# Kernel optimization log

Hardware: AMD Instinct MI355X
Metric: run time of the kernel (lower is better)

The kernel has to match this reference:

```python
import jax, jax.numpy as jnp
import numpy as np

EMBED_DIM = 768

def setup_inputs() -> dict:
    key = jax.random.key(0)
    ks = jax.random.split(key, 5)
    C = EMBED_DIM
    x = jax.random.normal(ks[0], (32, 1024, C), dtype=jnp.float32)
    s = 1.0 / np.sqrt(C)
    W_qkv = jax.random.normal(ks[1], (C, 3 * C), dtype=jnp.float32) * s
    b_qkv = jnp.zeros((3 * C,), dtype=jnp.float32)
    W_proj = jax.random.normal(ks[2], (C, C), dtype=jnp.float32) * s
    b_proj = jnp.zeros((C,), dtype=jnp.float32)
    return {"x": x, "W_qkv": W_qkv, "b_qkv": b_qkv, "W_proj": W_proj, "b_proj": b_proj}

def reference(x, W_qkv, b_qkv, W_proj, b_proj):
    B, N, C = x.shape
    qkv = x @ W_qkv + b_qkv                      # [B, N, 3C]
    q, k, v = jnp.split(qkv, 3, axis=-1)         # each [B, N, C]
    scale = 1.0 / jnp.sqrt(jnp.asarray(C, dtype=x.dtype))
    attn = jnp.einsum('bnc,bmc->bnm', q, k) * scale  # [B, N, N]
    attn = jax.nn.softmax(attn, axis=-1)
    out = jnp.einsum('bnm,bmc->bnc', attn, v)    # [B, N, C]
    return out @ W_proj + b_proj
```

## Files before the change

### kernel.cpp

```cpp
#include <hip/hip_runtime.h>

typedef __bf16 bf16;
typedef __bf16 bf16x4 __attribute__((ext_vector_type(4)));
typedef __bf16 bf16x8 __attribute__((ext_vector_type(8)));
typedef float f32x4 __attribute__((ext_vector_type(4)));

constexpr int BATCH = 32;
constexpr int SEQ   = 1024;
constexpr int CDIM  = 768;
constexpr int ROWS  = BATCH * SEQ;
constexpr int QKVC  = 3 * CDIM;

constexpr size_t oWqT = 0;
constexpr size_t oWpT = oWqT + (size_t)QKVC * CDIM * 2;
constexpr size_t oQKV = oWpT + (size_t)CDIM * CDIM * 2;
constexpr size_t oS   = oQKV + (size_t)ROWS * QKVC * 2;
constexpr size_t oVT  = oS   + (size_t)BATCH * SEQ * SEQ * 2;
constexpr size_t oInv = oVT  + (size_t)BATCH * CDIM * SEQ * 2;
constexpr size_t oAO  = oQKV;
constexpr size_t oXB  = oS;
constexpr size_t oPart= oWqT;

__device__ __forceinline__ void gld_lds16(const void* g, void* l) {
  __builtin_amdgcn_global_load_lds(
      (const __attribute__((address_space(1))) unsigned int*)g,
      (__attribute__((address_space(3))) unsigned int*)l,
      16, 0, 0);
}

__global__ __launch_bounds__(256) void f2b_kernel(const float* __restrict__ x,
                                                  bf16* __restrict__ y) {
  int i = blockIdx.x * blockDim.x + threadIdx.x;
  const float* p = x + (size_t)i * 8;
  float4 a = *(const float4*)p;
  float4 b = *(const float4*)(p + 4);
  bf16x8 o;
  o[0]=(bf16)a.x; o[1]=(bf16)a.y; o[2]=(bf16)a.z; o[3]=(bf16)a.w;
  o[4]=(bf16)b.x; o[5]=(bf16)b.y; o[6]=(bf16)b.z; o[7]=(bf16)b.w;
  *(bf16x8*)(y + (size_t)i * 8) = o;
}

__global__ __launch_bounds__(256) void wt_kernel(const float* __restrict__ W,
                                                 bf16* __restrict__ T, int N) {
  __shared__ float t[32][33];
  int k0 = blockIdx.x * 32, n0 = blockIdx.y * 32;
  int tx = threadIdx.x & 31, ty = threadIdx.x >> 5;
  #pragma unroll
  for (int i = 0; i < 4; ++i)
    t[ty + i * 8][tx] = W[(size_t)(k0 + ty + i * 8) * N + n0 + tx];
  __syncthreads();
  #pragma unroll
  for (int i = 0; i < 4; ++i)
    T[(size_t)(n0 + ty + i * 8) * 768 + k0 + tx] = (bf16)t[tx][ty + i * 8];
}

__global__ __launch_bounds__(256) void finish_kernel(const float* __restrict__ partial,
                                                     float* __restrict__ inv) {
  int i = blockIdx.x * 256 + threadIdx.x;
  float4 p = *(const float4*)(partial + (size_t)i * 4);
  inv[i] = 1.0f / (p.x + p.y + p.z + p.w);
}


#define DSRD_A(dst_, qm_) do {                                                   \
  _Pragma("unroll")                                                              \
  for (int i_ = 0; i_ < 4; ++i_) {                                               \
    const int row_ = wm * 128 + (qm_) * 64 + i_ * 16 + lr;                       \
    const char* rb_ = (const char*)Acur + row_ * 128;                            \
    dst_[i_][0] = *(const bf16x8*)(rb_ + ((0  + kb0) ^ swz));                    \
    dst_[i_][1] = *(const bf16x8*)(rb_ + ((64 + kb0) ^ swz));                    \
  }                                                                              \
} while (0)

#define DSRD_B(dst_, qn_) do {                                                   \
  _Pragma("unroll")                                                              \
  for (int j_ = 0; j_ < 2; ++j_) {                                               \
    const int row_ = wn * 64 + (qn_) * 32 + j_ * 16 + lr;                        \
    const char* rb_ = (const char*)Bcur + row_ * 128;                            \
    dst_[j_][0] = *(const bf16x8*)(rb_ + ((0  + kb0) ^ swz));                    \
    dst_[j_][1] = *(const bf16x8*)(rb_ + ((64 + kb0) ^ swz));                    \
  }                                                                              \
} while (0)

#define STG_A(buf_, kt_, h_) do {                                                \
  gld_lds16(Ast + (size_t)((h_) * 128 +  0) * lda + (size_t)(kt_) * 64,          \
            &LDSB[(buf_)][((h_) * 2 + 0) * 4096 + wv * 512]);                    \
  gld_lds16(Ast + (size_t)((h_) * 128 + 64) * lda + (size_t)(kt_) * 64,          \
            &LDSB[(buf_)][((h_) * 2 + 1) * 4096 + wv * 512]);                    \
} while (0)

#define STG_B(buf_, kt_, h_) do {                                                \
  gld_lds16(Bst + (size_t)((h_) * 128 +  0) * ldb + (size_t)(kt_) * 64,          \
            &LDSB[2 + (buf_)][((h_) * 2 + 0) * 4096 + wv * 512]);                \
  gld_lds16(Bst + (size_t)((h_) * 128 + 64) * ldb + (size_t)(kt_) * 64,          \
            &LDSB[2 + (buf_)][((h_) * 2 + 1) * 4096 + wv * 512]);                \
} while (0)

#define MMA16(a_, b_, mo_, no_) do {                                             \
  asm volatile("s_waitcnt lgkmcnt(0)" ::: "memory");                             \
  __builtin_amdgcn_sched_barrier(0);                                             \
  __builtin_amdgcn_s_setprio(1);                                                 \
  _Pragma("unroll")                                                              \
  for (int ks_ = 0; ks_ < 2; ++ks_)                                              \
    _Pragma("unroll")                                                            \
    for (int i_ = 0; i_ < 4; ++i_)                                               \
      _Pragma("unroll")                                                          \
      for (int j_ = 0; j_ < 2; ++j_)                                             \
        acc[(mo_) + i_][(no_) + j_] =                                            \
            __builtin_amdgcn_mfma_f32_16x16x32_bf16(a_[i_][ks_], b_[j_][ks_],    \
                acc[(mo_) + i_][(no_) + j_], 0, 0, 0);                           \
  __builtin_amdgcn_s_setprio(0);                                                 \
} while (0)

#define PIN() __builtin_amdgcn_sched_barrier(0)
#define BAR() __builtin_amdgcn_s_barrier()

template<bool OUT_BF16, bool HAS_BIAS, bool ROW_SCALE, bool FUSE_EXP, bool TR_V>
__global__ __launch_bounds__(512, 2) void gemm256(
    const bf16* __restrict__ Ap, const bf16* __restrict__ Bp, void* __restrict__ Cp,
    int K, int lda, int ldb, int ldc, int ntm, int ntn,
    long sA, long sB, long sC,
    float scale, const float* __restrict__ rowScale, long sRS,
    const float* __restrict__ bias, float* __restrict__ partial,
    bf16* __restrict__ vtout)
{
  __shared__ __align__(16) bf16 LDSB[4][256 * 64];
  const int tid  = threadIdx.x;
  const int lane = tid & 63;
  const int wv   = tid >> 6;
  const int wm   = wv >> 2;
  const int wn   = wv & 3;

  const int total = (int)gridDim.x;
  const int chunk = total >> 3;
  const int bid   = (int)blockIdx.x;
  int sbid = (bid & 7) * chunk + (bid >> 3);
  const int pb = ntm * ntn;
  const int z  = sbid / pb;  sbid -= z * pb;
  const int mt = sbid / ntn;
  const int nt = sbid - mt * ntn;
  const int m0 = mt * 256, n0 = nt * 256;

  const bf16* A = Ap + (size_t)z * sA;
  const bf16* B = Bp + (size_t)z * sB;

  const int sr  = tid >> 3;
  const int sc8 = tid & 7;
  const int gch = sc8 ^ (sr & 7);
  const bf16* Ast = A + (size_t)(m0 + sr) * lda + gch * 8;
  const bf16* Bst = B + (size_t)(n0 + sr) * ldb + gch * 8;

  const int lr  = lane & 15;
  const int swz = (lane & 7) << 4;
  const int kb0 = (lane >> 4) * 16;

  f32x4 acc[8][4] = {};
  const int nkt = K >> 6;

  STG_A(0, 0, 0); STG_A(0, 0, 1);
  STG_B(0, 0, 0); STG_B(0, 0, 1);
  if (nkt > 1) { STG_A(1, 1, 0); STG_A(1, 1, 1); }

  bf16x8 a0[4][2], a1[4][2], b0[2][2], b1[2][2];
  for (int t = 0; t < nkt; ++t) {
    const int cur = t & 1;
    const bf16* Acur = LDSB[cur];
    const bf16* Bcur = LDSB[2 + cur];
    const bool sb = (t + 1 < nkt);
    const bool sa = (t + 2 < nkt);
    if (sa) asm volatile("s_waitcnt vmcnt(4)" ::: "memory");
    else    asm volatile("s_waitcnt vmcnt(0)" ::: "memory");
    BAR(); PIN();
    DSRD_A(a0, 0); DSRD_B(b0, 0);
    PIN();
    if (sb) STG_B(cur ^ 1, t + 1, 0);
    MMA16(a0, b0, 0, 0);
    DSRD_A(a1, 1);
    PIN();
    if (sb) STG_B(cur ^ 1, t + 1, 1);
    MMA16(a1, b0, 4, 0);
    BAR(); PIN();
    DSRD_B(b1, 1);
    PIN();
    if (sa) STG_A(cur, t + 2, 0);
    MMA16(a1, b1, 4, 2);
    if (sa) STG_A(cur, t + 2, 1);
    PIN();
    MMA16(a0, b1, 0, 2);
  }

  if (TR_V && nt >= 6) {
    bf16* tile = LDSB[0];
    __syncthreads();
    #pragma unroll
    for (int mf = 0; mf < 8; ++mf) {
      #pragma unroll
      for (int nf = 0; nf < 4; ++nf) {
        const int lm = wm * 128 + mf * 16 + (lane >> 4) * 4;
        const int lc = wn * 64 + nf * 16 + (lane & 15);
        bf16x4 w;
        #pragma unroll
        for (int r = 0; r < 4; ++r) {
          float v = acc[mf][nf][r] * scale;
          if (HAS_BIAS) v += bias[n0 + lc];
          w[r] = (bf16)v;
        }
        *(bf16x4*)((char*)tile + lc * 512 + ((lm * 2) ^ ((lc & 7) << 4))) = w;
      }
    }
    __syncthreads();
    const int bz = m0 >> 10;
    const int mb = m0 & 1023;
    bf16* dst = vtout + ((size_t)bz * CDIM + (n0 - 2 * CDIM)) * SEQ + mb;
    #pragma unroll
    for (int it = 0; it < 16; ++it) {
      const int c  = (tid >> 5) + it * 16;
      const int ch = tid & 31;
      bf16x8 vv = *(const bf16x8*)((const char*)tile + c * 512 + ((ch * 16) ^ ((c & 7) << 4)));
      *(bf16x8*)(dst + (size_t)c * SEQ + ch * 8) = vv;
    }
  } else if (FUSE_EXP) {
    float rs[8][4];
    #pragma unroll
    for (int mf = 0; mf < 8; ++mf)
      #pragma unroll
      for (int r = 0; r < 4; ++r) rs[mf][r] = 0.f;
    #pragma unroll
    for (int mf = 0; mf < 8; ++mf)
      #pragma unroll
      for (int nf = 0; nf < 4; ++nf)
        #pragma unroll
        for (int r = 0; r < 4; ++r) {
          int gm = m0 + wm * 128 + mf * 16 + ((lane >> 4) * 4 + r);
          int gn = n0 + wn * 64 + nf * 16 + (lane & 15);
          float e = __expf(acc[mf][nf][r] * scale);
          ((bf16*)Cp)[(size_t)z * sC + (size_t)gm * ldc + gn] = (bf16)e;
          rs[mf][r] += e;
        }
    float* sl = (float*)LDSB;
    __syncthreads();
    #pragma unroll
    for (int mf = 0; mf < 8; ++mf)
      #pragma unroll
      for (int r = 0; r < 4; ++r) {
        float s = rs[mf][r];
        s += __shfl_xor(s, 1); s += __shfl_xor(s, 2);
        s += __shfl_xor(s, 4); s += __shfl_xor(s, 8);
        if ((lane & 15) == 0)
          sl[wn * 256 + wm * 128 + mf * 16 + (lane >> 4) * 4 + r] = s;
      }
    __syncthreads();
    if (tid < 256) {
      float s = sl[tid] + sl[256 + tid] + sl[512 + tid] + sl[768 + tid];
      partial[((size_t)z * SEQ + m0 + tid) * 4 + nt] = s;
    }
  } else {
    #pragma unroll
    for (int mf = 0; mf < 8; ++mf) {
      #pragma unroll
      for (int nf = 0; nf < 4; ++nf) {
        #pragma unroll
        for (int r = 0; r < 4; ++r) {
          int gm = m0 + wm * 128 + mf * 16 + ((lane >> 4) * 4 + r);
          int gn = n0 + wn * 64 + nf * 16 + (lane & 15);
          float v = acc[mf][nf][r] * scale;
          if (ROW_SCALE) v *= rowScale[(size_t)z * sRS + gm];
          if (HAS_BIAS)  v += bias[gn];
          if (OUT_BF16) ((bf16*)Cp)[(size_t)z * sC + (size_t)gm * ldc + gn] = (bf16)v;
          else          ((float*)Cp)[(size_t)z * sC + (size_t)gm * ldc + gn] = v;
        }
      }
    }
  }
}

extern "C" void kernel_launch(void* const* d_in, const int* in_sizes, int n_in,
                              void* d_out, int out_size, void* d_ws, size_t ws_size,
                              hipStream_t stream) {
  const float* x     = (const float*)d_in[0];
  const float* Wqkv  = (const float*)d_in[1];
  const float* bqkv  = (const float*)d_in[2];
  const float* Wproj = (const float*)d_in[3];
  const float* bproj = (const float*)d_in[4];
  float* out = (float*)d_out;
  char*  ws  = (char*)d_ws;

  bf16*  WqT = (bf16*)(ws + oWqT);
  bf16*  WpT = (bf16*)(ws + oWpT);
  bf16*  qkv = (bf16*)(ws + oQKV);
  bf16*  S   = (bf16*)(ws + oS);
  bf16*  VT  = (bf16*)(ws + oVT);
  float* inv = (float*)(ws + oInv);
  bf16*  AO  = (bf16*)(ws + oAO);
  bf16*  xb  = (bf16*)(ws + oXB);
  float* part= (float*)(ws + oPart);

  const float qk_scale = 1.0f / sqrtf((float)CDIM);

  f2b_kernel<<<ROWS * CDIM / 8 / 256, 256, 0, stream>>>(x, xb);
  wt_kernel<<<dim3(768 / 32, QKVC / 32), 256, 0, stream>>>(Wqkv, WqT, QKVC);
  wt_kernel<<<dim3(768 / 32, CDIM / 32), 256, 0, stream>>>(Wproj, WpT, CDIM);

  gemm256<true, true, false, false, true><<<(ROWS / 256) * (QKVC / 256), 512, 0, stream>>>(
      xb, WqT, qkv, CDIM, CDIM, CDIM, QKVC, ROWS / 256, QKVC / 256,
      0, 0, 0, 1.0f, nullptr, 0, bqkv, nullptr, VT);

  gemm256<true, false, false, true, false><<<BATCH * (SEQ / 256) * (SEQ / 256), 512, 0, stream>>>(
      qkv, qkv + CDIM, S, CDIM, QKVC, QKVC, SEQ, SEQ / 256, SEQ / 256,
      (long)SEQ * QKVC, (long)SEQ * QKVC, (long)SEQ * SEQ, qk_scale, nullptr, 0, nullptr, part, nullptr);

  finish_kernel<<<ROWS / 256, 256, 0, stream>>>(part, inv);

  gemm256<true, false, true, false, false><<<BATCH * (SEQ / 256) * (CDIM / 256), 512, 0, stream>>>(
      S, VT, AO, SEQ, SEQ, SEQ, CDIM, SEQ / 256, CDIM / 256,
      (long)SEQ * SEQ, (long)CDIM * SEQ, (long)SEQ * CDIM, 1.0f, inv, SEQ, nullptr, nullptr, nullptr);

  gemm256<false, true, false, false, false><<<(ROWS / 256) * (CDIM / 256), 512, 0, stream>>>(
      AO, WpT, out, CDIM, CDIM, CDIM, CDIM, ROWS / 256, CDIM / 256,
      0, 0, 0, 1.0f, nullptr, 0, bproj, nullptr, nullptr);
}
```

Baseline: 349.6 us.

## Unroll 256-tile GEMM main loop by two and use 128-tile GEMM for PV and projection

The 256x256 GEMM loop is unrolled by two so the LDS buffer indices are compile-time constants, and its wait counts are tuned per half-iteration. The PV and output-projection GEMMs move to a new simpler 128x128-tile kernel with 256 threads and a single-buffered LDS. The goal is better occupancy and wave count for those two GEMMs, which produced few tiles at 256. The cost is lower data reuse and no load/compute overlap in the new kernel.

```diff
diff --git a/kernel.cpp b/kernel.cpp
--- a/kernel.cpp
+++ b/kernel.cpp
@@ -114,14 +114,14 @@
 
 #define PIN() __builtin_amdgcn_sched_barrier(0)
 #define BAR() __builtin_amdgcn_s_barrier()
-
-template<bool OUT_BF16, bool HAS_BIAS, bool ROW_SCALE, bool FUSE_EXP, bool TR_V>
-__global__ __launch_bounds__(512, 2) void gemm256(
+#define WAITV(n_) asm volatile("s_waitcnt vmcnt(" #n_ ")" ::: "memory")
+
+template<bool OUT_BF16, bool HAS_BIAS, bool FUSE_EXP, bool TR_V>
+__global__ __launch_bounds__(512, 2) void gemm256d(
     const bf16* __restrict__ Ap, const bf16* __restrict__ Bp, void* __restrict__ Cp,
     int K, int lda, int ldb, int ldc, int ntm, int ntn,
     long sA, long sB, long sC,
-    float scale, const float* __restrict__ rowScale, long sRS,
-    const float* __restrict__ bias, float* __restrict__ partial,
+    float scale, const float* __restrict__ bias, float* __restrict__ partial,
     bf16* __restrict__ vtout)
 {
   __shared__ __align__(16) bf16 LDSB[4][256 * 64];
@@ -145,48 +145,64 @@
   const bf16* B = Bp + (size_t)z * sB;
 
   const int sr  = tid >> 3;
-  const int sc8 = tid & 7;
-  const int gch = sc8 ^ (sr & 7);
+  const int gch = (tid & 7) ^ (sr & 7);
   const bf16* Ast = A + (size_t)(m0 + sr) * lda + gch * 8;
   const bf16* Bst = B + (size_t)(n0 + sr) * ldb + gch * 8;
 
   const int lr  = lane & 15;
+  const int hi  = lane >> 4;
   const int swz = (lane & 7) << 4;
-  const int kb0 = (lane >> 4) * 16;
+  const int kb0 = hi * 16;
 
   f32x4 acc[8][4] = {};
   const int nkt = K >> 6;
 
   STG_A(0, 0, 0); STG_A(0, 0, 1);
   STG_B(0, 0, 0); STG_B(0, 0, 1);
-  if (nkt > 1) { STG_A(1, 1, 0); STG_A(1, 1, 1); }
+  STG_A(1, 1, 0); STG_A(1, 1, 1);
 
   bf16x8 a0[4][2], a1[4][2], b0[2][2], b1[2][2];
-  for (int t = 0; t < nkt; ++t) {
-    const int cur = t & 1;
-    const bf16* Acur = LDSB[cur];
-    const bf16* Bcur = LDSB[2 + cur];
-    const bool sb = (t + 1 < nkt);
-    const bool sa = (t + 2 < nkt);
-    if (sa) asm volatile("s_waitcnt vmcnt(4)" ::: "memory");
-    else    asm volatile("s_waitcnt vmcnt(0)" ::: "memory");
-    BAR(); PIN();
-    DSRD_A(a0, 0); DSRD_B(b0, 0);
-    PIN();
-    if (sb) STG_B(cur ^ 1, t + 1, 0);
-    MMA16(a0, b0, 0, 0);
-    DSRD_A(a1, 1);
-    PIN();
-    if (sb) STG_B(cur ^ 1, t + 1, 1);
-    MMA16(a1, b0, 4, 0);
-    BAR(); PIN();
-    DSRD_B(b1, 1);
-    PIN();
-    if (sa) STG_A(cur, t + 2, 0);
-    MMA16(a1, b1, 4, 2);
-    if (sa) STG_A(cur, t + 2, 1);
-    PIN();
-    MMA16(a0, b1, 0, 2);
+  for (int T = 0; T < nkt; T += 2) {
+    const bool sa = (T + 2 < nkt);
+    {
+      const bf16* Acur = LDSB[0];
+      const bf16* Bcur = LDSB[2];
+      WAITV(6); BAR(); PIN();
+      DSRD_A(a0, 0); DSRD_B(b0, 0);
+      PIN();
+      STG_B(1, T + 1, 0); STG_B(1, T + 1, 1);
+      MMA16(a0, b0, 0, 0);
+      DSRD_A(a1, 1); PIN();
+      MMA16(a1, b0, 4, 0);
+      WAITV(8); BAR(); PIN();
+      DSRD_B(b1, 1); PIN();
+      if (sa) STG_A(0, T + 2, 0);
+      MMA16(a1, b1, 4, 2);
+      if (sa) STG_A(0, T + 2, 1);
+      PIN();
+      MMA16(a0, b1, 0, 2);
+    }
+    {
+      const bf16* Acur = LDSB[1];
+      const bf16* Bcur = LDSB[3];
+      if (sa) { WAITV(6); } else { WAITV(2); }
+      BAR(); PIN();
+      DSRD_A(a0, 0); DSRD_B(b0, 0);
+      PIN();
+      if (sa) STG_B(0, T + 2, 0);
+      MMA16(a0, b0, 0, 0);
+      DSRD_A(a1, 1); PIN();
+      if (sa) STG_B(0, T + 2, 1);
+      MMA16(a1, b0, 4, 0);
+      if (sa) { WAITV(8); } else { WAITV(0); }
+      BAR(); PIN();
+      DSRD_B(b1, 1); PIN();
+      if (sa) STG_A(1, T + 3, 0);
+      MMA16(a1, b1, 4, 2);
+      if (sa) STG_A(1, T + 3, 1);
+      PIN();
+      MMA16(a0, b1, 0, 2);
+    }
   }
 
   if (TR_V && nt >= 6) {
@@ -196,8 +212,8 @@
     for (int mf = 0; mf < 8; ++mf) {
       #pragma unroll
       for (int nf = 0; nf < 4; ++nf) {
-        const int lm = wm * 128 + mf * 16 + (lane >> 4) * 4;
-        const int lc = wn * 64 + nf * 16 + (lane & 15);
+        const int lm = wm * 128 + mf * 16 + hi * 4;
+        const int lc = wn * 64 + nf * 16 + lr;
         bf16x4 w;
         #pragma unroll
         for (int r = 0; r < 4; ++r) {
@@ -231,8 +247,8 @@
       for (int nf = 0; nf < 4; ++nf)
         #pragma unroll
         for (int r = 0; r < 4; ++r) {
-          int gm = m0 + wm * 128 + mf * 16 + ((lane >> 4) * 4 + r);
-          int gn = n0 + wn * 64 + nf * 16 + (lane & 15);
+          int gm = m0 + wm * 128 + mf * 16 + hi * 4 + r;
+          int gn = n0 + wn * 64 + nf * 16 + lr;
           float e = __expf(acc[mf][nf][r] * scale);
           ((bf16*)Cp)[(size_t)z * sC + (size_t)gm * ldc + gn] = (bf16)e;
           rs[mf][r] += e;
@@ -246,8 +262,8 @@
         float s = rs[mf][r];
         s += __shfl_xor(s, 1); s += __shfl_xor(s, 2);
         s += __shfl_xor(s, 4); s += __shfl_xor(s, 8);
-        if ((lane & 15) == 0)
-          sl[wn * 256 + wm * 128 + mf * 16 + (lane >> 4) * 4 + r] = s;
+        if (lr == 0)
+          sl[wn * 256 + wm * 128 + mf * 16 + hi * 4 + r] = s;
       }
     __syncthreads();
     if (tid < 256) {
@@ -261,14 +277,99 @@
       for (int nf = 0; nf < 4; ++nf) {
         #pragma unroll
         for (int r = 0; r < 4; ++r) {
-          int gm = m0 + wm * 128 + mf * 16 + ((lane >> 4) * 4 + r);
-          int gn = n0 + wn * 64 + nf * 16 + (lane & 15);
+          int gm = m0 + wm * 128 + mf * 16 + hi * 4 + r;
+          int gn = n0 + wn * 64 + nf * 16 + lr;
           float v = acc[mf][nf][r] * scale;
-          if (ROW_SCALE) v *= rowScale[(size_t)z * sRS + gm];
-          if (HAS_BIAS)  v += bias[gn];
+          if (HAS_BIAS) v += bias[gn];
           if (OUT_BF16) ((bf16*)Cp)[(size_t)z * sC + (size_t)gm * ldc + gn] = (bf16)v;
           else          ((float*)Cp)[(size_t)z * sC + (size_t)gm * ldc + gn] = v;
         }
+      }
+    }
+  }
+}
+
+template<bool OUT_BF16, bool HAS_BIAS, bool ROW_SCALE>
+__global__ __launch_bounds__(256, 3) void gemm128(
+    const bf16* __restrict__ Ap, const bf16* __restrict__ Bp, void* __restrict__ Cp,
+    int K, int lda, int ldb, int ldc, int ntm, int ntn,
+    long sA, long sB, long sC,
+    float scale, const float* __restrict__ rowScale, long sRS,
+    const float* __restrict__ bias)
+{
+  __shared__ __align__(16) bf16 LDS[128 * 128];
+  bf16* As = LDS;
+  bf16* Bs = LDS + 128 * 64;
+  const int tid  = threadIdx.x;
+  const int lane = tid & 63;
+  const int wv   = tid >> 6;
+  const int wm   = wv >> 1;
+  const int wn   = wv & 1;
+
+  const int total = (int)gridDim.x;
+  const int chunk = total >> 3;
+  const int bid   = (int)blockIdx.x;
+  int sbid = (bid & 7) * chunk + (bid >> 3);
+  const int pb = ntm * ntn;
+  const int z  = sbid / pb;  sbid -= z * pb;
+  const int mt = sbid / ntn;
+  const int nt = sbid - mt * ntn;
+  const int m0 = mt * 128, n0 = nt * 128;
+
+  const bf16* A = Ap + (size_t)z * sA;
+  const bf16* B = Bp + (size_t)z * sB;
+
+  const int sr  = tid >> 3;
+  const int gch = (tid & 7) ^ (sr & 7);
+  const bf16* Ast = A + (size_t)(m0 + sr) * lda + gch * 8;
+  const bf16* Bst = B + (size_t)(n0 + sr) * ldb + gch * 8;
+
+  const int lr  = lane & 15;
+  const int hi  = lane >> 4;
+  const int swz = (lane & 7) << 4;
+  const int kb0 = hi * 16;
+
+  f32x4 acc[4][4] = {};
+
+  for (int kt = 0; kt < K; kt += 64) {
+    #pragma unroll
+    for (int it = 0; it < 4; ++it) {
+      gld_lds16(Ast + (size_t)(it * 32) * lda + kt, As + it * 2048 + wv * 512);
+      gld_lds16(Bst + (size_t)(it * 32) * ldb + kt, Bs + it * 2048 + wv * 512);
+    }
+    __syncthreads();
+    #pragma unroll
+    for (int ks = 0; ks < 2; ++ks) {
+      bf16x8 af[4], bfr[4];
+      #pragma unroll
+      for (int i = 0; i < 4; ++i) {
+        const int rm = wm * 64 + i * 16 + lr;
+        af[i]  = *(const bf16x8*)((const char*)As + rm * 128 + ((ks * 64 + kb0) ^ swz));
+        const int rn = wn * 64 + i * 16 + lr;
+        bfr[i] = *(const bf16x8*)((const char*)Bs + rn * 128 + ((ks * 64 + kb0) ^ swz));
+      }
+      #pragma unroll
+      for (int i = 0; i < 4; ++i)
+        #pragma unroll
+        for (int j = 0; j < 4; ++j)
+          acc[i][j] = __builtin_amdgcn_mfma_f32_16x16x32_bf16(af[i], bfr[j], acc[i][j], 0, 0, 0);
+    }
+    __syncthreads();
+  }
+
+  #pragma unroll
+  for (int i = 0; i < 4; ++i) {
+    #pragma unroll
+    for (int j = 0; j < 4; ++j) {
+      #pragma unroll
+      for (int r = 0; r < 4; ++r) {
+        const int gm = m0 + wm * 64 + i * 16 + hi * 4 + r;
+        const int gn = n0 + wn * 64 + j * 16 + lr;
+        float v = acc[i][j][r] * scale;
+        if (ROW_SCALE) v *= rowScale[(size_t)z * sRS + gm];
+        if (HAS_BIAS)  v += bias[gn];
+        if (OUT_BF16) ((bf16*)Cp)[(size_t)z * sC + (size_t)gm * ldc + gn] = (bf16)v;
+        else          ((float*)Cp)[(size_t)z * sC + (size_t)gm * ldc + gn] = v;
       }
     }
   }
@@ -301,21 +402,21 @@
   wt_kernel<<<dim3(768 / 32, QKVC / 32), 256, 0, stream>>>(Wqkv, WqT, QKVC);
   wt_kernel<<<dim3(768 / 32, CDIM / 32), 256, 0, stream>>>(Wproj, WpT, CDIM);
 
-  gemm256<true, true, false, false, true><<<(ROWS / 256) * (QKVC / 256), 512, 0, stream>>>(
+  gemm256d<true, true, false, true><<<(ROWS / 256) * (QKVC / 256), 512, 0, stream>>>(
       xb, WqT, qkv, CDIM, CDIM, CDIM, QKVC, ROWS / 256, QKVC / 256,
-      0, 0, 0, 1.0f, nullptr, 0, bqkv, nullptr, VT);
-
-  gemm256<true, false, false, true, false><<<BATCH * (SEQ / 256) * (SEQ / 256), 512, 0, stream>>>(
+      0, 0, 0, 1.0f, bqkv, nullptr, VT);
+
+  gemm256d<true, false, true, false><<<BATCH * (SEQ / 256) * (SEQ / 256), 512, 0, stream>>>(
       qkv, qkv + CDIM, S, CDIM, QKVC, QKVC, SEQ, SEQ / 256, SEQ / 256,
-      (long)SEQ * QKVC, (long)SEQ * QKVC, (long)SEQ * SEQ, qk_scale, nullptr, 0, nullptr, part, nullptr);
+      (long)SEQ * QKVC, (long)SEQ * QKVC, (long)SEQ * SEQ, qk_scale, nullptr, part, nullptr);
 
   finish_kernel<<<ROWS / 256, 256, 0, stream>>>(part, inv);
 
-  gemm256<true, false, true, false, false><<<BATCH * (SEQ / 256) * (CDIM / 256), 512, 0, stream>>>(
-      S, VT, AO, SEQ, SEQ, SEQ, CDIM, SEQ / 256, CDIM / 256,
-      (long)SEQ * SEQ, (long)CDIM * SEQ, (long)SEQ * CDIM, 1.0f, inv, SEQ, nullptr, nullptr, nullptr);
-
-  gemm256<false, true, false, false, false><<<(ROWS / 256) * (CDIM / 256), 512, 0, stream>>>(
-      AO, WpT, out, CDIM, CDIM, CDIM, CDIM, ROWS / 256, CDIM / 256,
-      0, 0, 0, 1.0f, nullptr, 0, bproj, nullptr, nullptr);
-}
+  gemm128<true, false, true><<<BATCH * (SEQ / 128) * (CDIM / 128), 256, 0, stream>>>(
+      S, VT, AO, SEQ, SEQ, SEQ, CDIM, SEQ / 128, CDIM / 128,
+      (long)SEQ * SEQ, (long)CDIM * SEQ, (long)SEQ * CDIM, 1.0f, inv, SEQ, nullptr);
+
+  gemm128<false, true, false><<<(ROWS / 128) * (CDIM / 128), 256, 0, stream>>>(
+      AO, WpT, out, CDIM, CDIM, CDIM, CDIM, ROWS / 128, CDIM / 128,
+      0, 0, 0, 1.0f, nullptr, 0, bproj);
+}
```

After: 417.8 us. +19.5%, slower.
